# Kernel tuning notes

Measured on AMD Instinct MI355X. Metric: run time of the kernel, lower is better.

## Reference

```python
import jax, jax.numpy as jnp
import numpy as np

TOP_K = 2
EPS = 1e-9

def setup_inputs() -> dict:
    key = jax.random.key(0)
    ks = jax.random.split(key, 8)
    B, L, C, F = 64, 512, 3, 300          # batteries, cycles, channels, curve length
    d_model, d_llm, d_ff, E = 512, 4096, 2048, 8
    s = lambda k, sh: jax.random.normal(k, sh, jnp.float32) * 0.02
    return dict(
        cycle_curve_data=jax.random.normal(ks[0], (B, L, C, F), jnp.float32),
        cycle_numbers=jax.random.uniform(ks[1], (B, 1), jnp.float32),
        DKP_embeddings=jax.random.normal(ks[2], (B, d_llm), jnp.float32),
        gate_W1=s(ks[3], (d_llm + 1, d_ff)), gate_b1=jnp.zeros((d_ff,), jnp.float32),
        gate_W2=s(ks[4], (d_ff, E)), gate_b2=jnp.zeros((E,), jnp.float32),
        expert_W=s(ks[5], (E, C * F, d_model)), expert_b=jnp.zeros((E, d_model), jnp.float32),
        gen_W=s(ks[6], (C * F, d_model)), gen_b=jnp.zeros((d_model,), jnp.float32),
    )

def reference(cycle_curve_data, cycle_numbers, DKP_embeddings,
              gate_W1, gate_b1, gate_W2, gate_b2,
              expert_W, expert_b, gen_W, gen_b):
    B, L, C, F = cycle_curve_data.shape
    # router (PatternRouter_two): 2-layer MLP over [DKP embedding ; cycle number]
    g_in = jnp.concatenate([DKP_embeddings, cycle_numbers], axis=-1)   # [B, d_llm+1]
    h = jax.nn.gelu(g_in @ gate_W1 + gate_b1)
    logits = h @ gate_W2 + gate_b2                                     # [B, E]
    # top-k mask on raw logits (as in source), softmax, mask, renormalize
    _, idx = jax.lax.top_k(logits, TOP_K)
    mask = jnp.zeros(logits.shape, bool).at[jnp.arange(B)[:, None], idx].set(True)
    p = jax.nn.softmax(logits, axis=1)
    g = jnp.where(mask, p, 0.0)
    gates = g / (jnp.sum(g, axis=1, keepdims=True) + EPS)              # [B, E]
    # experts: flatten(start_dim=2) then Linear(3*F -> d_model); combine is linear
    # so fold gates into a per-battery weight: sum_e gates[b,e] * W_e
    x = cycle_curve_data.reshape(B, L, C * F)                          # [B, L, 3F]
    Wb = jnp.einsum('be,eid->bid', gates, expert_W)                    # [B, 3F, d]
    bb = gates @ expert_b                                              # [B, d]
    moe_out = jnp.einsum('bli,bid->bld', x, Wb) + bb[:, None, :]       # [B, L, d]
    general = x @ gen_W + gen_b                                        # [B, L, d]
    # source casts the combined MoE output to bf16 before adding
    return general + moe_out.astype(jnp.bfloat16)
```

## Files before the change

kernel.cpp:

```cpp
#include <hip/hip_runtime.h>
#include <hip/hip_bf16.h>
#include <stdint.h>

typedef __attribute__((ext_vector_type(8))) short short8;
typedef __attribute__((ext_vector_type(4))) short short4v;
typedef __attribute__((ext_vector_type(4))) float f32x4;

__device__ inline unsigned short f2bf(float f) {
    union { float f; uint32_t u; } v; v.f = f;
    uint32_t u = v.u;
    uint32_t r = (u + 0x7FFFu + ((u >> 16) & 1u)) >> 16;
    return (unsigned short)r;
}

__device__ inline short4v pk4(float4 a) {
    short4v r;
    r[0] = (short)f2bf(a.x); r[1] = (short)f2bf(a.y);
    r[2] = (short)f2bf(a.z); r[3] = (short)f2bf(a.w);
    return r;
}

__global__ __launch_bounds__(256) void router1(const float* __restrict__ DKP,
                                               const float* __restrict__ W1,
                                               float* __restrict__ part) {
    __shared__ float gin[16 * 64];
    const int t  = threadIdx.x;
    const int bg = blockIdx.x & 3, jc = blockIdx.x >> 2;
    const int ks = blockIdx.y;
    const int k0 = ks * 64;
    {
        const int b = t >> 4, q = t & 15;
        *(float4*)(gin + b * 64 + q * 4) =
            *(const float4*)(DKP + (size_t)(bg * 16 + b) * 4096 + k0 + q * 4);
    }
    __syncthreads();
    const int ja = jc * 512 + t, jb = ja + 256;
    float accA[16], accB[16];
    #pragma unroll
    for (int b = 0; b < 16; ++b) { accA[b] = 0.f; accB[b] = 0.f; }
    #pragma unroll 1
    for (int oct = 0; oct < 8; ++oct) {
        const int kk = oct * 8;
        float wa[8], wb[8];
        #pragma unroll
        for (int i = 0; i < 8; ++i) {
            const float* wr = W1 + (size_t)(k0 + kk + i) * 2048;
            wa[i] = wr[ja]; wb[i] = wr[jb];
        }
        #pragma unroll
        for (int b = 0; b < 16; ++b) {
            float4 g0 = *(const float4*)(gin + b * 64 + kk);
            float4 g1 = *(const float4*)(gin + b * 64 + kk + 4);
            accA[b] += g0.x*wa[0] + g0.y*wa[1] + g0.z*wa[2] + g0.w*wa[3]
                     + g1.x*wa[4] + g1.y*wa[5] + g1.z*wa[6] + g1.w*wa[7];
            accB[b] += g0.x*wb[0] + g0.y*wb[1] + g0.z*wb[2] + g0.w*wb[3]
                     + g1.x*wb[4] + g1.y*wb[5] + g1.z*wb[6] + g1.w*wb[7];
        }
    }
    #pragma unroll 1
    for (int b = 0; b < 16; ++b) {
        const size_t row = (size_t)(ks * 64 + bg * 16 + b) * 2048;
        part[row + ja] = accA[b];
        part[row + jb] = accB[b];
    }
}

__global__ __launch_bounds__(256) void router2(const float* __restrict__ part,
                                               const float* __restrict__ cyc,
                                               const float* __restrict__ W1,
                                               const float* __restrict__ b1,
                                               float* __restrict__ h) {
    const int idx = blockIdx.x * 256 + threadIdx.x;
    const int j = idx & 2047, b = idx >> 11;
    float s = 0.f;
    #pragma unroll 8
    for (int t = 0; t < 64; ++t)
        s += part[((size_t)t * 64 + b) * 2048 + j];
    s += cyc[b] * W1[(size_t)4096 * 2048 + j] + b1[j];
    const float u  = s + 0.044715f * s * s * s;
    const float th = tanhf(0.7978845608028654f * u);
    h[idx] = 0.5f * s * (1.0f + th);
}

__global__ __launch_bounds__(256) void router3(const float* __restrict__ h,
                                               const float* __restrict__ W2,
                                               const float* __restrict__ b2,
                                               float4* __restrict__ gates) {
    __shared__ float red[256 * 8];
    __shared__ float lg[8];
    const int b = blockIdx.x, t = threadIdx.x;
    float acc[8];
    #pragma unroll
    for (int e = 0; e < 8; ++e) acc[e] = 0.f;
    for (int k = t; k < 2048; k += 256) {
        const float hv = h[(size_t)b * 2048 + k];
        const float* w = W2 + (size_t)k * 8;
        #pragma unroll
        for (int e = 0; e < 8; ++e) acc[e] += hv * w[e];
    }
    #pragma unroll
    for (int e = 0; e < 8; ++e) red[t * 8 + e] = acc[e];
    __syncthreads();
    if (t < 8) {
        float s = 0.f;
        for (int r = 0; r < 256; ++r) s += red[r * 8 + t];
        lg[t] = s + b2[t];
    }
    __syncthreads();
    if (t == 0) {
        float l[8];
        #pragma unroll
        for (int e = 0; e < 8; ++e) l[e] = lg[e];
        int e0 = 0;
        #pragma unroll
        for (int e = 1; e < 8; ++e) if (l[e] > l[e0]) e0 = e;
        int e1 = (e0 == 0) ? 1 : 0;
        #pragma unroll
        for (int e = 0; e < 8; ++e) if (e != e0 && l[e] > l[e1]) e1 = e;
        const float m = l[e0];
        float p[8], Z = 0.f;
        #pragma unroll
        for (int e = 0; e < 8; ++e) { p[e] = expf(l[e] - m); Z += p[e]; }
        const float pe0 = p[e0] / Z, pe1 = p[e1] / Z;
        const float s2 = pe0 + pe1 + 1e-9f;
        gates[b] = make_float4(__int_as_float(e0), __int_as_float(e1), pe0 / s2, pe1 / s2);
    }
}

__global__ __launch_bounds__(256) void combine_w(const float* __restrict__ genW,
                                                 const float* __restrict__ expW,
                                                 const float4* __restrict__ gates,
                                                 unsigned short* __restrict__ wc) {
    __shared__ unsigned short T[64 * 72];
    const int b  = blockIdx.z;
    const int i0 = blockIdx.y * 64;
    const int d0 = blockIdx.x * 64;
    const float4 gt = gates[b];
    const int e0 = __float_as_int(gt.x), e1 = __float_as_int(gt.y);
    const float g0 = gt.z, g1 = gt.w;
    const float* W0 = expW + (size_t)e0 * 900 * 512;
    const float* W1e = expW + (size_t)e1 * 900 * 512;
    const int t = threadIdx.x;
    {
        const int il = t >> 2, c = t & 3;
        const int i = i0 + il;
        const bool valid = (i < 900);
        const size_t rowoff = (size_t)i * 512 + d0 + c * 16;
        #pragma unroll
        for (int s = 0; s < 4; ++s) {
            float4 g  = valid ? *(const float4*)(genW + rowoff + 4 * s) : make_float4(0,0,0,0);
            float4 w0 = valid ? *(const float4*)(W0   + rowoff + 4 * s) : make_float4(0,0,0,0);
            float4 w1 = valid ? *(const float4*)(W1e  + rowoff + 4 * s) : make_float4(0,0,0,0);
            const int dl = c * 16 + 4 * s;
            T[(dl + 0) * 72 + il] = f2bf(g.x + g0 * w0.x + g1 * w1.x);
            T[(dl + 1) * 72 + il] = f2bf(g.y + g0 * w0.y + g1 * w1.y);
            T[(dl + 2) * 72 + il] = f2bf(g.z + g0 * w0.z + g1 * w1.z);
            T[(dl + 3) * 72 + il] = f2bf(g.w + g0 * w0.w + g1 * w1.w);
        }
    }
    __syncthreads();
    {
        const int dl = t >> 2, seg = t & 3;
        const int ic = seg * 16;
        if (i0 + ic < 928) {
            short8 v0 = *(const short8*)&T[dl * 72 + ic];
            short8 v1 = *(const short8*)&T[dl * 72 + ic + 8];
            unsigned short* dst = wc + (size_t)b * 512 * 928 + (size_t)(d0 + dl) * 928 + i0 + ic;
            *(short8*)dst = v0;
            *((short8*)dst + 1) = v1;
        }
    }
}

__global__ __launch_bounds__(512, 4) void moe_gemm(const float* __restrict__ x,
                                                   const unsigned short* __restrict__ wc,
                                                   const float4* __restrict__ gates,
                                                   const float* __restrict__ eb,
                                                   const float* __restrict__ genb,
                                                   float* __restrict__ out) {
    __shared__ unsigned short As[64 * 40];
    __shared__ unsigned short Bs[512 * 32];
    const int b  = blockIdx.x;
    const int m0 = blockIdx.y * 64;
    const int t = threadIdx.x, lane = t & 63, wid = t >> 6;
    const float4 gt = gates[b];
    const int e0 = __float_as_int(gt.x), e1 = __float_as_int(gt.y);
    const float g0 = gt.z, g1 = gt.w;
    const float* xb = x + (size_t)b * 512 * 900;
    const unsigned short* wcb = wc + (size_t)b * 512 * 928;
    f32x4 acc[4][4];
    #pragma unroll
    for (int mi = 0; mi < 4; ++mi)
        #pragma unroll
        for (int ni = 0; ni < 4; ++ni)
            acc[mi][ni] = (f32x4){0.f, 0.f, 0.f, 0.f};

    const int arow  = t >> 3;
    const int akoff = (t & 7) * 4;
    const float* xrow = xb + (size_t)(m0 + arow) * 900 + akoff;
    const int bseg = (lane & 3) ^ ((lane >> 3) & 3);
    const int burow = lane >> 2;

    const int wn = wid * 64;
    const int lm = lane & 15, lq = lane >> 4;

    for (int kt = 0; kt < 29; ++kt) {
        const int k0 = kt * 32;
        #pragma unroll
        for (int r = 0; r < 4; ++r) {
            const int chunk = wid * 4 + r;
            const int n = chunk * 16 + burow;
            const unsigned short* gsrc = wcb + (size_t)n * 928 + k0 + bseg * 8;
            unsigned short* ldst = &Bs[chunk * 512];
            __builtin_amdgcn_global_load_lds(
                (const __attribute__((address_space(1))) unsigned int*)gsrc,
                (__attribute__((address_space(3))) unsigned int*)ldst, 16, 0, 0);
        }
        float4 f;
        if (k0 + 32 <= 900) {
            f = *(const float4*)(xrow + k0);
        } else {
            float v[4];
            #pragma unroll
            for (int i = 0; i < 4; ++i) {
                const int k = k0 + akoff + i;
                v[i] = (k < 900) ? xrow[k0 + i] : 0.f;
            }
            f = make_float4(v[0], v[1], v[2], v[3]);
        }
        *(short4v*)&As[arow * 40 + akoff] = pk4(f);
        __syncthreads();
        short8 af[4], bf[4];
        #pragma unroll
        for (int mi = 0; mi < 4; ++mi)
            af[mi] = *(const short8*)&As[(mi * 16 + lm) * 40 + lq * 8];
        #pragma unroll
        for (int ni = 0; ni < 4; ++ni) {
            const int n = wn + ni * 16 + lm;
            const int slot = lq ^ ((lm >> 1) & 3);
            bf[ni] = *(const short8*)&Bs[n * 32 + slot * 8];
        }
        #pragma unroll
        for (int mi = 0; mi < 4; ++mi)
            #pragma unroll
            for (int ni = 0; ni < 4; ++ni)
                acc[mi][ni] = __builtin_amdgcn_mfma_f32_16x16x32_bf16(
                    af[mi], bf[ni], acc[mi][ni], 0, 0, 0);
        __syncthreads();
    }
    #pragma unroll
    for (int ni = 0; ni < 4; ++ni) {
        const int col = wn + ni * 16 + lm;
        const float bias = genb[col] + g0 * eb[e0 * 512 + col] + g1 * eb[e1 * 512 + col];
        #pragma unroll
        for (int mi = 0; mi < 4; ++mi) {
            const int row = m0 + mi * 16 + lq * 4;
            #pragma unroll
            for (int r = 0; r < 4; ++r)
                out[((size_t)b * 512 + row + r) * 512 + col] = acc[mi][ni][r] + bias;
        }
    }
}

extern "C" void kernel_launch(void* const* d_in, const int* in_sizes, int n_in,
                              void* d_out, int out_size, void* d_ws, size_t ws_size,
                              hipStream_t stream) {
    const float* x    = (const float*)d_in[0];
    const float* cyc  = (const float*)d_in[1];
    const float* dkp  = (const float*)d_in[2];
    const float* gW1  = (const float*)d_in[3];
    const float* gb1  = (const float*)d_in[4];
    const float* gW2  = (const float*)d_in[5];
    const float* gb2  = (const float*)d_in[6];
    const float* eW   = (const float*)d_in[7];
    const float* eb   = (const float*)d_in[8];
    const float* genW = (const float*)d_in[9];
    const float* genb = (const float*)d_in[10];
    float* out = (float*)d_out;

    char* ws = (char*)d_ws;
    unsigned short* wcomb = (unsigned short*)ws;
    float* part  = (float*)ws;
    float* h     = (float*)(ws + 60817408);
    float4* gts  = (float4*)(ws + 60817408 + 524288);

    router1<<<dim3(16, 64), 256, 0, stream>>>(dkp, gW1, part);
    router2<<<512, 256, 0, stream>>>(part, cyc, gW1, gb1, h);
    router3<<<64, 256, 0, stream>>>(h, gW2, gb2, gts);
    combine_w<<<dim3(8, 15, 64), 256, 0, stream>>>(genW, eW, gts, wcomb);
    moe_gemm<<<dim3(64, 8), 512, 0, stream>>>(x, wcomb, gts, eb, genb, out);
}
```

Measured before the change: 400.0 us.

## Pre-swizzle combined weights into MFMA fragment layout and stage full x rows in LDS

combine_w now writes the per-battery combined weight directly in MFMA B-fragment order, so moe_gemm can load B operands straight from global memory into registers with double buffering and no LDS staging or per-tile barriers. moe_gemm now converts a whole 32-row x slab to bf16 in LDS up front and uses 256-thread blocks, each computing 32 rows by 512 columns. router1 drops its shared-memory staging: each thread keeps 64 batch accumulators and reads DKP straight from global memory. The trade-offs are heavy register pressure from the 64 router accumulators and the B fragments, and strided, uncoalesced reads in combine_w.

```diff
diff --git a/kernel.cpp b/kernel.cpp
--- a/kernel.cpp
+++ b/kernel.cpp
@@ -20,49 +20,34 @@
     return r;
 }
 
-__global__ __launch_bounds__(256) void router1(const float* __restrict__ DKP,
+__global__ __launch_bounds__(512) void router1(const float* __restrict__ DKP,
                                                const float* __restrict__ W1,
                                                float* __restrict__ part) {
-    __shared__ float gin[16 * 64];
     const int t  = threadIdx.x;
-    const int bg = blockIdx.x & 3, jc = blockIdx.x >> 2;
+    const int jc = blockIdx.x;
     const int ks = blockIdx.y;
     const int k0 = ks * 64;
-    {
-        const int b = t >> 4, q = t & 15;
-        *(float4*)(gin + b * 64 + q * 4) =
-            *(const float4*)(DKP + (size_t)(bg * 16 + b) * 4096 + k0 + q * 4);
-    }
-    __syncthreads();
-    const int ja = jc * 512 + t, jb = ja + 256;
-    float accA[16], accB[16];
-    #pragma unroll
-    for (int b = 0; b < 16; ++b) { accA[b] = 0.f; accB[b] = 0.f; }
+    const int j  = jc * 512 + t;
+    float acc[64];
+    #pragma unroll
+    for (int b = 0; b < 64; ++b) acc[b] = 0.f;
     #pragma unroll 1
     for (int oct = 0; oct < 8; ++oct) {
-        const int kk = oct * 8;
-        float wa[8], wb[8];
-        #pragma unroll
-        for (int i = 0; i < 8; ++i) {
-            const float* wr = W1 + (size_t)(k0 + kk + i) * 2048;
-            wa[i] = wr[ja]; wb[i] = wr[jb];
-        }
-        #pragma unroll
-        for (int b = 0; b < 16; ++b) {
-            float4 g0 = *(const float4*)(gin + b * 64 + kk);
-            float4 g1 = *(const float4*)(gin + b * 64 + kk + 4);
-            accA[b] += g0.x*wa[0] + g0.y*wa[1] + g0.z*wa[2] + g0.w*wa[3]
-                     + g1.x*wa[4] + g1.y*wa[5] + g1.z*wa[6] + g1.w*wa[7];
-            accB[b] += g0.x*wb[0] + g0.y*wb[1] + g0.z*wb[2] + g0.w*wb[3]
-                     + g1.x*wb[4] + g1.y*wb[5] + g1.z*wb[6] + g1.w*wb[7];
+        const int kk = k0 + oct * 8;
+        float w[8];
+        #pragma unroll
+        for (int i = 0; i < 8; ++i)
+            w[i] = W1[(size_t)(kk + i) * 2048 + j];
+        #pragma unroll
+        for (int b = 0; b < 64; ++b) {
+            const float* dk = DKP + (size_t)b * 4096 + kk;
+            acc[b] += dk[0]*w[0] + dk[1]*w[1] + dk[2]*w[2] + dk[3]*w[3]
+                    + dk[4]*w[4] + dk[5]*w[5] + dk[6]*w[6] + dk[7]*w[7];
         }
     }
     #pragma unroll 1
-    for (int b = 0; b < 16; ++b) {
-        const size_t row = (size_t)(ks * 64 + bg * 16 + b) * 2048;
-        part[row + ja] = accA[b];
-        part[row + jb] = accB[b];
-    }
+    for (int b = 0; b < 64; ++b)
+        part[(size_t)(ks * 64 + b) * 2048 + j] = acc[b];
 }
 
 __global__ __launch_bounds__(256) void router2(const float* __restrict__ part,
@@ -131,133 +116,115 @@
                                                  const float* __restrict__ expW,
                                                  const float4* __restrict__ gates,
                                                  unsigned short* __restrict__ wc) {
-    __shared__ unsigned short T[64 * 72];
-    const int b  = blockIdx.z;
-    const int i0 = blockIdx.y * 64;
-    const int d0 = blockIdx.x * 64;
+    const int b  = blockIdx.x;
+    const int kc = blockIdx.y;
     const float4 gt = gates[b];
     const int e0 = __float_as_int(gt.x), e1 = __float_as_int(gt.y);
     const float g0 = gt.z, g1 = gt.w;
-    const float* W0 = expW + (size_t)e0 * 900 * 512;
+    const float* W0  = expW + (size_t)e0 * 900 * 512;
     const float* W1e = expW + (size_t)e1 * 900 * 512;
-    const int t = threadIdx.x;
-    {
-        const int il = t >> 2, c = t & 3;
-        const int i = i0 + il;
-        const bool valid = (i < 900);
-        const size_t rowoff = (size_t)i * 512 + d0 + c * 16;
-        #pragma unroll
-        for (int s = 0; s < 4; ++s) {
-            float4 g  = valid ? *(const float4*)(genW + rowoff + 4 * s) : make_float4(0,0,0,0);
-            float4 w0 = valid ? *(const float4*)(W0   + rowoff + 4 * s) : make_float4(0,0,0,0);
-            float4 w1 = valid ? *(const float4*)(W1e  + rowoff + 4 * s) : make_float4(0,0,0,0);
-            const int dl = c * 16 + 4 * s;
-            T[(dl + 0) * 72 + il] = f2bf(g.x + g0 * w0.x + g1 * w1.x);
-            T[(dl + 1) * 72 + il] = f2bf(g.y + g0 * w0.y + g1 * w1.y);
-            T[(dl + 2) * 72 + il] = f2bf(g.z + g0 * w0.z + g1 * w1.z);
-            T[(dl + 3) * 72 + il] = f2bf(g.w + g0 * w0.w + g1 * w1.w);
-        }
-    }
-    __syncthreads();
-    {
-        const int dl = t >> 2, seg = t & 3;
-        const int ic = seg * 16;
-        if (i0 + ic < 928) {
-            short8 v0 = *(const short8*)&T[dl * 72 + ic];
-            short8 v1 = *(const short8*)&T[dl * 72 + ic + 8];
-            unsigned short* dst = wc + (size_t)b * 512 * 928 + (size_t)(d0 + dl) * 928 + i0 + ic;
-            *(short8*)dst = v0;
-            *((short8*)dst + 1) = v1;
-        }
-    }
-}
-
-__global__ __launch_bounds__(512, 4) void moe_gemm(const float* __restrict__ x,
+    const int t = threadIdx.x, l = t & 63, w = t >> 6;
+    const int lm = l & 15, lq = l >> 4;
+    unsigned short* outb = wc + (size_t)b * 32 * 29 * 512;
+    #pragma unroll
+    for (int q = 0; q < 8; ++q) {
+        const int nb = w * 8 + q;
+        const int n  = nb * 16 + lm;
+        short8 v;
+        #pragma unroll
+        for (int j = 0; j < 8; ++j) {
+            const int k = kc * 32 + lq * 8 + j;
+            float f = 0.f;
+            if (k < 900) {
+                const size_t o = (size_t)k * 512 + n;
+                f = genW[o] + g0 * W0[o] + g1 * W1e[o];
+            }
+            v[j] = (short)f2bf(f);
+        }
+        *(short8*)(outb + (size_t)(nb * 29 + kc) * 512 + l * 8) = v;
+    }
+}
+
+__global__ __launch_bounds__(256, 2) void moe_gemm(const float* __restrict__ x,
                                                    const unsigned short* __restrict__ wc,
                                                    const float4* __restrict__ gates,
                                                    const float* __restrict__ eb,
                                                    const float* __restrict__ genb,
                                                    float* __restrict__ out) {
-    __shared__ unsigned short As[64 * 40];
-    __shared__ unsigned short Bs[512 * 32];
+    __shared__ unsigned short As[32 * 936];
     const int b  = blockIdx.x;
-    const int m0 = blockIdx.y * 64;
+    const int m0 = blockIdx.y * 32;
     const int t = threadIdx.x, lane = t & 63, wid = t >> 6;
+    {
+        const int r = t >> 3, s = t & 7;
+        const float* xrow = x + ((size_t)b * 512 + m0 + r) * 900;
+        unsigned short* arow = As + r * 936;
+        for (int c = s * 4; c < 900; c += 32)
+            *(short4v*)(arow + c) = pk4(*(const float4*)(xrow + c));
+        if (s < 7) *(short4v*)(arow + 900 + s * 4) = (short4v){0, 0, 0, 0};
+    }
     const float4 gt = gates[b];
     const int e0 = __float_as_int(gt.x), e1 = __float_as_int(gt.y);
     const float g0 = gt.z, g1 = gt.w;
-    const float* xb = x + (size_t)b * 512 * 900;
-    const unsigned short* wcb = wc + (size_t)b * 512 * 928;
-    f32x4 acc[4][4];
-    #pragma unroll
-    for (int mi = 0; mi < 4; ++mi)
-        #pragma unroll
-        for (int ni = 0; ni < 4; ++ni)
-            acc[mi][ni] = (f32x4){0.f, 0.f, 0.f, 0.f};
-
-    const int arow  = t >> 3;
-    const int akoff = (t & 7) * 4;
-    const float* xrow = xb + (size_t)(m0 + arow) * 900 + akoff;
-    const int bseg = (lane & 3) ^ ((lane >> 3) & 3);
-    const int burow = lane >> 2;
-
-    const int wn = wid * 64;
+    const unsigned short* wcb = wc + (size_t)b * 32 * 29 * 512;
+    const unsigned short* bptr[8];
+    #pragma unroll
+    for (int q = 0; q < 8; ++q)
+        bptr[q] = wcb + (size_t)((wid * 8 + q) * 29) * 512 + lane * 8;
+    short8 B0[8], B1[8];
+    #pragma unroll
+    for (int q = 0; q < 8; ++q) B0[q] = *(const short8*)(bptr[q]);
+    #pragma unroll
+    for (int q = 0; q < 8; ++q) B1[q] = *(const short8*)(bptr[q] + 512);
+    __syncthreads();
     const int lm = lane & 15, lq = lane >> 4;
-
-    for (int kt = 0; kt < 29; ++kt) {
-        const int k0 = kt * 32;
-        #pragma unroll
-        for (int r = 0; r < 4; ++r) {
-            const int chunk = wid * 4 + r;
-            const int n = chunk * 16 + burow;
-            const unsigned short* gsrc = wcb + (size_t)n * 928 + k0 + bseg * 8;
-            unsigned short* ldst = &Bs[chunk * 512];
-            __builtin_amdgcn_global_load_lds(
-                (const __attribute__((address_space(1))) unsigned int*)gsrc,
-                (__attribute__((address_space(3))) unsigned int*)ldst, 16, 0, 0);
-        }
-        float4 f;
-        if (k0 + 32 <= 900) {
-            f = *(const float4*)(xrow + k0);
-        } else {
-            float v[4];
+    f32x4 acc[2][8];
+    #pragma unroll
+    for (int mi = 0; mi < 2; ++mi)
+        #pragma unroll
+        for (int q = 0; q < 8; ++q)
+            acc[mi][q] = (f32x4){0.f, 0.f, 0.f, 0.f};
+
+    #pragma unroll 1
+    for (int kt = 0; kt < 29; kt += 2) {
+        short8 af0, af1;
+        af0 = *(const short8*)&As[(lm)      * 936 + kt * 32 + lq * 8];
+        af1 = *(const short8*)&As[(16 + lm) * 936 + kt * 32 + lq * 8];
+        #pragma unroll
+        for (int q = 0; q < 8; ++q) {
+            acc[0][q] = __builtin_amdgcn_mfma_f32_16x16x32_bf16(af0, B0[q], acc[0][q], 0, 0, 0);
+            acc[1][q] = __builtin_amdgcn_mfma_f32_16x16x32_bf16(af1, B0[q], acc[1][q], 0, 0, 0);
+        }
+        if (kt + 2 < 29) {
             #pragma unroll
-            for (int i = 0; i < 4; ++i) {
-                const int k = k0 + akoff + i;
-                v[i] = (k < 900) ? xrow[k0 + i] : 0.f;
+            for (int q = 0; q < 8; ++q)
+                B0[q] = *(const short8*)(bptr[q] + (size_t)(kt + 2) * 512);
+        }
+        if (kt + 1 < 29) {
+            af0 = *(const short8*)&As[(lm)      * 936 + (kt + 1) * 32 + lq * 8];
+            af1 = *(const short8*)&As[(16 + lm) * 936 + (kt + 1) * 32 + lq * 8];
+            #pragma unroll
+            for (int q = 0; q < 8; ++q) {
+                acc[0][q] = __builtin_amdgcn_mfma_f32_16x16x32_bf16(af0, B1[q], acc[0][q], 0, 0, 0);
+                acc[1][q] = __builtin_amdgcn_mfma_f32_16x16x32_bf16(af1, B1[q], acc[1][q], 0, 0, 0);
             }
-            f = make_float4(v[0], v[1], v[2], v[3]);
-        }
-        *(short4v*)&As[arow * 40 + akoff] = pk4(f);
-        __syncthreads();
-        short8 af[4], bf[4];
-        #pragma unroll
-        for (int mi = 0; mi < 4; ++mi)
-            af[mi] = *(const short8*)&As[(mi * 16 + lm) * 40 + lq * 8];
-        #pragma unroll
-        for (int ni = 0; ni < 4; ++ni) {
-            const int n = wn + ni * 16 + lm;
-            const int slot = lq ^ ((lm >> 1) & 3);
-            bf[ni] = *(const short8*)&Bs[n * 32 + slot * 8];
-        }
-        #pragma unroll
-        for (int mi = 0; mi < 4; ++mi)
-            #pragma unroll
-            for (int ni = 0; ni < 4; ++ni)
-                acc[mi][ni] = __builtin_amdgcn_mfma_f32_16x16x32_bf16(
-                    af[mi], bf[ni], acc[mi][ni], 0, 0, 0);
-        __syncthreads();
-    }
-    #pragma unroll
-    for (int ni = 0; ni < 4; ++ni) {
-        const int col = wn + ni * 16 + lm;
+            if (kt + 3 < 29) {
+                #pragma unroll
+                for (int q = 0; q < 8; ++q)
+                    B1[q] = *(const short8*)(bptr[q] + (size_t)(kt + 3) * 512);
+            }
+        }
+    }
+    #pragma unroll
+    for (int q = 0; q < 8; ++q) {
+        const int col = wid * 128 + q * 16 + lm;
         const float bias = genb[col] + g0 * eb[e0 * 512 + col] + g1 * eb[e1 * 512 + col];
         #pragma unroll
-        for (int mi = 0; mi < 4; ++mi) {
+        for (int mi = 0; mi < 2; ++mi) {
             const int row = m0 + mi * 16 + lq * 4;
             #pragma unroll
             for (int r = 0; r < 4; ++r)
-                out[((size_t)b * 512 + row + r) * 512 + col] = acc[mi][ni][r] + bias;
+                out[((size_t)b * 512 + row + r) * 512 + col] = acc[mi][q][r] + bias;
         }
     }
 }
@@ -284,9 +251,9 @@
     float* h     = (float*)(ws + 60817408);
     float4* gts  = (float4*)(ws + 60817408 + 524288);
 
-    router1<<<dim3(16, 64), 256, 0, stream>>>(dkp, gW1, part);
+    router1<<<dim3(4, 64), 512, 0, stream>>>(dkp, gW1, part);
     router2<<<512, 256, 0, stream>>>(part, cyc, gW1, gb1, h);
     router3<<<64, 256, 0, stream>>>(h, gW2, gb2, gts);
-    combine_w<<<dim3(8, 15, 64), 256, 0, stream>>>(genW, eW, gts, wcomb);
-    moe_gemm<<<dim3(64, 8), 512, 0, stream>>>(x, wcomb, gts, eb, genb, out);
-}
+    combine_w<<<dim3(64, 29), 256, 0, stream>>>(genW, eW, gts, wcomb);
+    moe_gemm<<<dim3(64, 16), 256, 0, stream>>>(x, wcomb, gts, eb, genb, out);
+}
```

New measurement: 477.7 us. +19.4%, slower.
